# Kernel optimization log

Measured on AMD Instinct MI355X. Metric: run time of the kernel, lower is better.

## Reference

```python
import jax, jax.numpy as jnp
import numpy as np

C_IN, K_R, K_C, N_K = 32, 3, 3, 64
STRIDE = (1, 1)
PAD = (1, 1)


def setup_inputs() -> dict:
    key = jax.random.key(0)
    k1, k2, k3 = jax.random.split(key, 3)
    x = jax.random.normal(k1, (32, C_IN, 128, 128), dtype=jnp.float32)
    kernels = jax.random.normal(k2, (N_K, K_R * K_C * C_IN), dtype=jnp.float32) * 0.05
    bias = jax.random.normal(k3, (N_K, 1), dtype=jnp.float32) * 0.05
    return {"x": x, "kernels": kernels, "bias": bias}


def reference(x, kernels, bias):
    # kernels rows are [C, kr, kc] flattened (per-channel im2col blocks stacked
    # along dim 0 in the original unroll) -> OIHW conv weight.
    w = kernels.reshape(N_K, C_IN, K_R, K_C)
    out = jax.lax.conv_general_dilated(
        x, w,
        window_strides=STRIDE,
        padding=[(PAD[0], PAD[0]), (PAD[1], PAD[1])],
        dimension_numbers=("NCHW", "OIHW", "NCHW"),
    )
    # bias (K, 1) broadcast over all output positions
    return out + bias.reshape(1, N_K, 1, 1)
```

## Files before the change

### kernel.cpp

```cpp
#include <hip/hip_runtime.h>


typedef __attribute__((ext_vector_type(8))) short bf16x8;
typedef __attribute__((ext_vector_type(4))) float f32x4;

#define NB 32
#define CIN 32
#define HH 128
#define WW 128
#define NK 64

__device__ __forceinline__ unsigned short f2bf(float f) {
    union { float f; unsigned int u; } v; v.f = f;
    unsigned int u = v.u;
    return (unsigned short)((u + 0x7FFFu + ((u >> 16) & 1u)) >> 16);
}

__device__ __forceinline__ int xel(int wi, int c) {
    return wi * 32 + ((((c >> 3) ^ ((wi >> 2) & 3)) << 3) | (c & 7));
}
__device__ __forceinline__ int wel(int kidx, int ok, int c) {
    return (kidx * 64 + ok) * 32 + ((((c >> 3) ^ (ok & 3)) << 3) | (c & 7));
}

__global__ __launch_bounds__(256) void conv3x3_mfma(
        const float* __restrict__ x, const float* __restrict__ kern,
        const float* __restrict__ bias, float* __restrict__ out) {
    __shared__ unsigned short lds_w[9 * 64 * 32];
    __shared__ unsigned short lds_x[130 * 32];

    const int tid = threadIdx.x;
    const int h = blockIdx.x;
    const int n = blockIdx.y;
    const int lane = tid & 63;
    const int l16 = lane & 15;
    const int q = lane >> 4;
    const int wav = tid >> 6;
    const int ok_base = (wav & 1) * 32;
    const int w_base = (wav >> 1) * 64;

    {
        const float4* k4 = (const float4*)kern;
        #pragma unroll
        for (int i = 0; i < 18; ++i) {
            int u = tid + i * 256;
            float4 v = k4[u];
            int g = u * 4;
            #pragma unroll
            for (int j = 0; j < 4; ++j) {
                int gg = g + j;
                int ok = gg / 288;
                int rem = gg - ok * 288;
                int c = rem / 9;
                int kidx = rem - c * 9;
                lds_w[wel(kidx, ok, c)] = f2bf((&v.x)[j]);
            }
        }
    }
    if (tid < 64) {
        int c = tid & 31;
        int wi = (tid < 32) ? 0 : 129;
        lds_x[xel(wi, c)] = 0;
    }

    f32x4 acc[2][4];
    #pragma unroll
    for (int mi = 0; mi < 2; ++mi)
        #pragma unroll
        for (int ni = 0; ni < 4; ++ni)
            acc[mi][ni] = (f32x4){0.f, 0.f, 0.f, 0.f};

    for (int kr = 0; kr < 3; ++kr) {
        const int r = h + kr - 1;
        if (r < 0 || r >= HH) continue;
        __syncthreads();
        #pragma unroll
        for (int it = 0; it < 2; ++it) {
            int u = it * 256 + tid;
            int c = (u >> 5) * 2;
            int wq = u & 31;
            const float4* pa = (const float4*)(x + ((n * CIN + c) * HH + r) * WW) + wq;
            const float4* pb = (const float4*)(x + ((n * CIN + c + 1) * HH + r) * WW) + wq;
            float4 va = *pa;
            float4 vb = *pb;
            #pragma unroll
            for (int j = 0; j < 4; ++j) {
                int w = wq * 4 + j;
                unsigned int pk = (unsigned int)f2bf((&va.x)[j]) |
                                  ((unsigned int)f2bf((&vb.x)[j]) << 16);
                *(unsigned int*)&lds_x[xel(w + 1, c)] = pk;
            }
        }
        __syncthreads();
        #pragma unroll
        for (int kc = 0; kc < 3; ++kc) {
            const int kidx = kr * 3 + kc;
            bf16x8 afr[2];
            #pragma unroll
            for (int mi = 0; mi < 2; ++mi)
                afr[mi] = *(const bf16x8*)&lds_w[wel(kidx, ok_base + mi * 16 + l16, q * 8)];
            #pragma unroll
            for (int ni = 0; ni < 4; ++ni) {
                bf16x8 bfr = *(const bf16x8*)&lds_x[xel(w_base + ni * 16 + l16 + kc, q * 8)];
                #pragma unroll
                for (int mi = 0; mi < 2; ++mi)
                    acc[mi][ni] = __builtin_amdgcn_mfma_f32_16x16x32_bf16(
                        afr[mi], bfr, acc[mi][ni], 0, 0, 0);
            }
        }
    }

    #pragma unroll
    for (int mi = 0; mi < 2; ++mi) {
        #pragma unroll
        for (int rg = 0; rg < 4; ++rg) {
            int ok = ok_base + mi * 16 + q * 4 + rg;
            float bv = bias[ok];
            float* orow = out + ((size_t)(n * NK + ok) * HH + h) * WW;
            #pragma unroll
            for (int ni = 0; ni < 4; ++ni)
                orow[w_base + ni * 16 + l16] = acc[mi][ni][rg] + bv;
        }
    }
}

extern "C" void kernel_launch(void* const* d_in, const int* in_sizes, int n_in,
                              void* d_out, int out_size, void* d_ws, size_t ws_size,
                              hipStream_t stream) {
    const float* x    = (const float*)d_in[0];
    const float* kern = (const float*)d_in[1];
    const float* bias = (const float*)d_in[2];
    float* out = (float*)d_out;
    dim3 grid(HH, NB);
    conv3x3_mfma<<<grid, 256, 0, stream>>>(x, kern, bias, out);
}
```

Before: 214.2 us.

## Pre-repack weights into MFMA fragment layout and load all three input rows upfront

A separate small kernel converts the weights to bf16 once per call, writing them in MFMA fragment order to workspace. The conv kernel then reads A fragments directly from global/L2 instead of converting and staging 36KB of weights into LDS in every block. All three input rows are loaded into LDS together before a single barrier, replacing the per-row load/sync loop. It also remaps the row index for locality and sets an occupancy hint. The costs are an extra kernel launch and weight reads from global memory inside the MFMA loop.

```diff
diff --git a/kernel.cpp b/kernel.cpp
--- a/kernel.cpp
+++ b/kernel.cpp
@@ -1,4 +1,5 @@
 #include <hip/hip_runtime.h>
+#include <hip/hip_bf16.h>
 
 
 typedef __attribute__((ext_vector_type(8))) short bf16x8;
@@ -9,6 +10,7 @@
 #define HH 128
 #define WW 128
 #define NK 64
+#define XROW (130 * 32)
 
 __device__ __forceinline__ unsigned short f2bf(float f) {
     union { float f; unsigned int u; } v; v.f = f;
@@ -19,49 +21,69 @@
 __device__ __forceinline__ int xel(int wi, int c) {
     return wi * 32 + ((((c >> 3) ^ ((wi >> 2) & 3)) << 3) | (c & 7));
 }
-__device__ __forceinline__ int wel(int kidx, int ok, int c) {
-    return (kidx * 64 + ok) * 32 + ((((c >> 3) ^ (ok & 3)) << 3) | (c & 7));
+
+__global__ void repack_w(const float* __restrict__ kern,
+                         unsigned short* __restrict__ wfrag) {
+    int u = blockIdx.x * 256 + threadIdx.x;
+    int j = u & 7;
+    int lane = (u >> 3) & 63;
+    int tile = (u >> 9) & 3;
+    int kidx = u >> 11;
+    int ok = tile * 16 + (lane & 15);
+    int c = ((lane >> 4) << 3) + j;
+    wfrag[u] = f2bf(kern[ok * 288 + c * 9 + kidx]);
 }
 
-__global__ __launch_bounds__(256) void conv3x3_mfma(
-        const float* __restrict__ x, const float* __restrict__ kern,
+__global__ __launch_bounds__(256, 4) void conv3x3_mfma(
+        const float* __restrict__ x, const unsigned short* __restrict__ wfrag,
         const float* __restrict__ bias, float* __restrict__ out) {
-    __shared__ unsigned short lds_w[9 * 64 * 32];
-    __shared__ unsigned short lds_x[130 * 32];
+    __shared__ unsigned short lds_x[3 * XROW];
 
     const int tid = threadIdx.x;
-    const int h = blockIdx.x;
+    const int bx = blockIdx.x;
+    const int h = ((bx & 7) << 4) | (bx >> 3);
     const int n = blockIdx.y;
     const int lane = tid & 63;
     const int l16 = lane & 15;
     const int q = lane >> 4;
     const int wav = tid >> 6;
-    const int ok_base = (wav & 1) * 32;
+    const int ok_tile = (wav & 1) * 2;
     const int w_base = (wav >> 1) * 64;
 
-    {
-        const float4* k4 = (const float4*)kern;
+    if (tid < 192) {
+        int kr = tid >> 6;
+        int idx = tid & 63;
+        int c = idx & 31;
+        int wi = (idx < 32) ? 0 : 129;
+        lds_x[kr * XROW + xel(wi, c)] = 0;
+    }
+
+    #pragma unroll
+    for (int kr = 0; kr < 3; ++kr) {
+        const int r = h + kr - 1;
+        const bool valid = (unsigned)r < HH;
+        const float* xrow = x + ((size_t)(n * CIN) * HH + r) * WW;
+        unsigned short* lrow = lds_x + kr * XROW;
         #pragma unroll
-        for (int i = 0; i < 18; ++i) {
-            int u = tid + i * 256;
-            float4 v = k4[u];
-            int g = u * 4;
+        for (int it = 0; it < 2; ++it) {
+            int u = it * 256 + tid;
+            int c = (u >> 5) * 2;
+            int wq = u & 31;
+            float4 va = {0.f, 0.f, 0.f, 0.f}, vb = {0.f, 0.f, 0.f, 0.f};
+            if (valid) {
+                va = *((const float4*)(xrow + (size_t)c * HH * WW) + wq);
+                vb = *((const float4*)(xrow + (size_t)(c + 1) * HH * WW) + wq);
+            }
             #pragma unroll
             for (int j = 0; j < 4; ++j) {
-                int gg = g + j;
-                int ok = gg / 288;
-                int rem = gg - ok * 288;
-                int c = rem / 9;
-                int kidx = rem - c * 9;
-                lds_w[wel(kidx, ok, c)] = f2bf((&v.x)[j]);
+                int w = wq * 4 + j;
+                __hip_bfloat162 h2 = __float22bfloat162_rn(
+                    make_float2((&va.x)[j], (&vb.x)[j]));
+                *(unsigned int*)&lrow[xel(w + 1, c)] = *(unsigned int*)&h2;
             }
         }
     }
-    if (tid < 64) {
-        int c = tid & 31;
-        int wi = (tid < 32) ? 0 : 129;
-        lds_x[xel(wi, c)] = 0;
-    }
+    __syncthreads();
 
     f32x4 acc[2][4];
     #pragma unroll
@@ -70,38 +92,20 @@
         for (int ni = 0; ni < 4; ++ni)
             acc[mi][ni] = (f32x4){0.f, 0.f, 0.f, 0.f};
 
+    #pragma unroll 1
     for (int kr = 0; kr < 3; ++kr) {
-        const int r = h + kr - 1;
-        if (r < 0 || r >= HH) continue;
-        __syncthreads();
-        #pragma unroll
-        for (int it = 0; it < 2; ++it) {
-            int u = it * 256 + tid;
-            int c = (u >> 5) * 2;
-            int wq = u & 31;
-            const float4* pa = (const float4*)(x + ((n * CIN + c) * HH + r) * WW) + wq;
-            const float4* pb = (const float4*)(x + ((n * CIN + c + 1) * HH + r) * WW) + wq;
-            float4 va = *pa;
-            float4 vb = *pb;
-            #pragma unroll
-            for (int j = 0; j < 4; ++j) {
-                int w = wq * 4 + j;
-                unsigned int pk = (unsigned int)f2bf((&va.x)[j]) |
-                                  ((unsigned int)f2bf((&vb.x)[j]) << 16);
-                *(unsigned int*)&lds_x[xel(w + 1, c)] = pk;
-            }
-        }
-        __syncthreads();
+        const unsigned short* lrow = lds_x + kr * XROW;
         #pragma unroll
         for (int kc = 0; kc < 3; ++kc) {
             const int kidx = kr * 3 + kc;
             bf16x8 afr[2];
             #pragma unroll
             for (int mi = 0; mi < 2; ++mi)
-                afr[mi] = *(const bf16x8*)&lds_w[wel(kidx, ok_base + mi * 16 + l16, q * 8)];
+                afr[mi] = *(const bf16x8*)
+                    &wfrag[(size_t)(((kidx * 4) + ok_tile + mi) * 64 + lane) * 8];
             #pragma unroll
             for (int ni = 0; ni < 4; ++ni) {
-                bf16x8 bfr = *(const bf16x8*)&lds_x[xel(w_base + ni * 16 + l16 + kc, q * 8)];
+                bf16x8 bfr = *(const bf16x8*)&lrow[xel(w_base + ni * 16 + l16 + kc, q * 8)];
                 #pragma unroll
                 for (int mi = 0; mi < 2; ++mi)
                     acc[mi][ni] = __builtin_amdgcn_mfma_f32_16x16x32_bf16(
@@ -114,7 +118,7 @@
     for (int mi = 0; mi < 2; ++mi) {
         #pragma unroll
         for (int rg = 0; rg < 4; ++rg) {
-            int ok = ok_base + mi * 16 + q * 4 + rg;
+            int ok = (wav & 1) * 32 + mi * 16 + q * 4 + rg;
             float bv = bias[ok];
             float* orow = out + ((size_t)(n * NK + ok) * HH + h) * WW;
             #pragma unroll
@@ -131,6 +135,9 @@
     const float* kern = (const float*)d_in[1];
     const float* bias = (const float*)d_in[2];
     float* out = (float*)d_out;
+    unsigned short* wfrag = (unsigned short*)d_ws;
+
+    repack_w<<<72, 256, 0, stream>>>(kern, wfrag);
     dim3 grid(HH, NB);
-    conv3x3_mfma<<<grid, 256, 0, stream>>>(x, kern, bias, out);
+    conv3x3_mfma<<<grid, 256, 0, stream>>>(x, wfrag, bias, out);
 }
```

Result: faster. 197.7 us (-7.7%).
